# Kernel tuning notes

Measured on AMD Instinct MI355X. Metric: run time of the kernel, lower is better.

The kernel has to match this reference:

```python
import jax, jax.numpy as jnp
import numpy as np

E, K = 8, 2            # num_experts, top_k
H, DFF = 1024, 2048    # embd_dim, d_ff
B, S = 4, 1024


def setup_inputs() -> dict:
    key = jax.random.key(0)
    ks = jax.random.split(key, 5)
    s_in = 1.0 / np.sqrt(H)
    s_ff = 1.0 / np.sqrt(DFF)
    return {
        "x": jax.random.normal(ks[0], (B, S, H), jnp.float32),
        "centroids": jax.random.normal(ks[1], (E, H), jnp.float32),
        # nn.Linear weights are [out, in]
        "gate_w": jax.random.normal(ks[2], (E, DFF, H), jnp.float32) * s_in,
        "up_w": jax.random.normal(ks[3], (E, DFF, H), jnp.float32) * s_in,
        "down_w": jax.random.normal(ks[4], (E, H, DFF), jnp.float32) * s_ff,
        "routing_bias": jnp.zeros((E,), jnp.float32),
    }


def reference(x, centroids, gate_w, up_w, down_w, routing_bias):
    Bb, Ss, Hh = x.shape
    xf = x.reshape(-1, Hh)  # [T, H]
    # sigmoid affinity router + (non-trainable) routing bias
    affinity = jax.nn.sigmoid(xf @ centroids.T)          # [T, E]
    topk_scores, topk_idx = jax.lax.top_k(affinity + routing_bias, K)  # [T, K]
    topk_w = jax.nn.softmax(topk_scores, axis=-1)        # [T, K]

    # Dense per-expert SwiGLU FFN on all tokens (same math as the
    # sort/gather grouped loop; selection happens in the gather below).
    g = jnp.einsum('th,efh->etf', xf, gate_w)            # [E, T, DFF]
    u = jnp.einsum('th,efh->etf', xf, up_w)              # [E, T, DFF]
    y = jnp.einsum('etf,ehf->eth', jax.nn.silu(g) * u, down_w)  # [E, T, H]

    yt = jnp.transpose(y, (1, 0, 2))                     # [T, E, H]
    sel = jnp.take_along_axis(yt, topk_idx[:, :, None], axis=1)  # [T, K, H]
    out_flat = jnp.sum(sel * topk_w[:, :, None], axis=1)  # [T, H]

    counts = jnp.bincount(topk_idx.ravel(), length=E)    # per-expert token counts
    return out_flat.reshape(Bb, Ss, Hh), counts
```

## Files before the change

kernel.cpp:

```cpp
#include <hip/hip_runtime.h>
#include <math.h>

constexpr int E = 8, H = 1024, DFF = 2048, T = 4096;
constexpr int TR = 8192;
constexpr int MAXJ = 72;

typedef __bf16 bf16x8 __attribute__((ext_vector_type(8)));
typedef __bf16 bf16x4 __attribute__((ext_vector_type(4)));
typedef float f32x4 __attribute__((ext_vector_type(4)));

__device__ __forceinline__ void gload16(const void* g, void* l) {
    __builtin_amdgcn_global_load_lds(
        (const __attribute__((address_space(1))) unsigned int*)g,
        (__attribute__((address_space(3))) unsigned int*)l, 16, 0, 0);
}

__global__ __launch_bounds__(256) void k1_affinity(
    const float* __restrict__ x, const float* __restrict__ cent,
    const float* __restrict__ bias,
    int* __restrict__ se, float* __restrict__ sw) {
    __shared__ float cs[E * H];
    int tid = threadIdx.x;
    for (int i = tid; i < E * H / 4; i += 256)
        ((float4*)cs)[i] = ((const float4*)cent)[i];
    __syncthreads();

    int wave = tid >> 6, lane = tid & 63;
    int t = blockIdx.x * 4 + wave;
    const float4* xr = (const float4*)(x + (size_t)t * H);
    float acc[E] = {};
    #pragma unroll
    for (int it = 0; it < 4; it++) {
        float4 xv = xr[lane + it * 64];
        #pragma unroll
        for (int e = 0; e < E; e++) {
            float4 cv = ((const float4*)(cs + e * H))[lane + it * 64];
            acc[e] = fmaf(xv.x, cv.x, acc[e]);
            acc[e] = fmaf(xv.y, cv.y, acc[e]);
            acc[e] = fmaf(xv.z, cv.z, acc[e]);
            acc[e] = fmaf(xv.w, cv.w, acc[e]);
        }
    }
    #pragma unroll
    for (int off = 32; off; off >>= 1)
        #pragma unroll
        for (int e = 0; e < E; e++) acc[e] += __shfl_down(acc[e], off);

    if (lane == 0) {
        float s[E];
        #pragma unroll
        for (int e = 0; e < E; e++)
            s[e] = 1.0f / (1.0f + expf(-acc[e])) + bias[e];
        int i0 = 0;
        for (int e = 1; e < E; e++) if (s[e] > s[i0]) i0 = e;
        int i1 = -1;
        for (int e = 0; e < E; e++) {
            if (e == i0) continue;
            if (i1 < 0 || s[e] > s[i1]) i1 = e;
        }
        float m = fmaxf(s[i0], s[i1]);
        float w0 = expf(s[i0] - m), w1 = expf(s[i1] - m);
        float inv = 1.0f / (w0 + w1);
        se[2 * t] = i0;     sw[2 * t] = w0 * inv;
        se[2 * t + 1] = i1; sw[2 * t + 1] = w1 * inv;
    }
}

__global__ __launch_bounds__(256) void k1b_partition(
    const int* __restrict__ se, int* __restrict__ token_list,
    int* __restrict__ sp, int* __restrict__ cnt) {
    int e = blockIdx.x;
    int tid = threadIdx.x;
    int wave = tid >> 6, lane = tid & 63;
    __shared__ int wsum[4];
    int running = 0;
    for (int c0 = 0; c0 < 2 * T; c0 += 256) {
        int i = c0 + tid;
        bool pred = (se[i] == e);
        unsigned long long mask = __ballot(pred);
        int pos_in_wave = __popcll(mask & ((1ull << lane) - 1ull));
        if (lane == 0) wsum[wave] = __popcll(mask);
        __syncthreads();
        int wbase = 0;
        for (int w2 = 0; w2 < wave; w2++) wbase += wsum[w2];
        int total = wsum[0] + wsum[1] + wsum[2] + wsum[3];
        if (pred) {
            int p = running + wbase + pos_in_wave;
            token_list[e * T + p] = i >> 1;
            sp[i] = p;
        }
        running += total;
        __syncthreads();
    }
    if (tid == 0) cnt[e] = running;
}

__global__ void k15_offsets(const int* __restrict__ cnt, int* __restrict__ off,
                            float* __restrict__ out_counts,
                            int* __restrict__ jobs, int* __restrict__ njobs) {
    if (threadIdx.x == 0) {
        int acc = 0, nj = 0;
        for (int e = 0; e < E; e++) {
            off[e] = acc; acc += cnt[e];
            int mts = (cnt[e] + 127) >> 7;
            for (int mt = 0; mt < mts; mt++) jobs[nj++] = e * 64 + mt;
        }
        njobs[0] = nj;
    }
    if (threadIdx.x < E) out_counts[threadIdx.x] = (float)cnt[threadIdx.x];
}

__global__ __launch_bounds__(256) void k_conv(const float* __restrict__ in,
                                              __bf16* __restrict__ out, int n4) {
    int i = blockIdx.x * 256 + threadIdx.x;
    if (i < n4) {
        float4 v = ((const float4*)in)[i];
        bf16x4 o = {(__bf16)v.x, (__bf16)v.y, (__bf16)v.z, (__bf16)v.w};
        ((bf16x4*)out)[i] = o;
    }
}

__global__ __launch_bounds__(256) void k_conv3(
    const float* __restrict__ gw, __bf16* __restrict__ gwb,
    const float* __restrict__ uw, __bf16* __restrict__ uwb,
    const float* __restrict__ x, __bf16* __restrict__ xb,
    int w4, int x4) {
    int i = blockIdx.x * 256 + threadIdx.x;
    const float* in; __bf16* out; int idx;
    if (i < w4) { in = gw; out = gwb; idx = i; }
    else if (i < 2 * w4) { in = uw; out = uwb; idx = i - w4; }
    else { idx = i - 2 * w4; if (idx >= x4) return; in = x; out = xb; }
    float4 v = ((const float4*)in)[idx];
    bf16x4 o = {(__bf16)v.x, (__bf16)v.y, (__bf16)v.z, (__bf16)v.w};
    ((bf16x4*)out)[idx] = o;
}

__global__ __launch_bounds__(256, 2) void k2_gateup(
    const __bf16* __restrict__ xb, const __bf16* __restrict__ gwb,
    const __bf16* __restrict__ uwb, const int* __restrict__ cnt,
    const int* __restrict__ off, const int* __restrict__ token_list,
    const int* __restrict__ jobs, const int* __restrict__ njobs,
    __bf16* __restrict__ h) {
    int jt = blockIdx.x >> 4, nt = blockIdx.x & 15;
    if (jt >= njobs[0]) return;
    int job = jobs[jt];
    int e = job >> 6, mt = job & 63;
    int Me = cnt[e], offe = off[e];

    __shared__ __bf16 As[128 * 64];
    __shared__ __bf16 Bg[128 * 64];
    __shared__ __bf16 Bu[128 * 64];

    int tid = threadIdx.x;
    int lane = tid & 63, w = tid >> 6;
    int wm = w >> 1, wn = w & 1;

    const __bf16* asrc[4];
    const __bf16 *bsg[4], *bsu[4];
    #pragma unroll
    for (int rr = 0; rr < 4; rr++) {
        int l = rr * 256 + tid;
        int row = l >> 3, sl = l & 7;
        int gr = mt * 128 + row; if (gr >= Me) gr = Me - 1;
        int tok = token_list[e * T + gr];
        asrc[rr] = xb + (size_t)tok * H + ((sl ^ (row & 7)) * 8);
        size_t base = ((size_t)e * DFF + nt * 128 + row) * H + ((sl ^ (row & 7)) * 8);
        bsg[rr] = gwb + base;
        bsu[rr] = uwb + base;
    }

    f32x4 accg[4][4] = {};
    f32x4 accu[4][4] = {};
    int kq = lane >> 4, m15 = lane & 15;

    for (int k0 = 0; k0 < H; k0 += 64) {
        #pragma unroll
        for (int rr = 0; rr < 4; rr++) {
            gload16(asrc[rr] + k0, &As[(rr * 256 + tid) * 8]);
            gload16(bsg[rr] + k0, &Bg[(rr * 256 + tid) * 8]);
            gload16(bsu[rr] + k0, &Bu[(rr * 256 + tid) * 8]);
        }
        __syncthreads();

        #pragma unroll
        for (int kc = 0; kc < 2; kc++) {
            bf16x8 af[4], gf[4], uf[4];
            #pragma unroll
            for (int i = 0; i < 4; i++) {
                int row = wm * 64 + i * 16 + m15;
                int sl = (kc * 4 + kq) ^ (row & 7);
                af[i] = *(const bf16x8*)&As[row * 64 + sl * 8];
            }
            #pragma unroll
            for (int j = 0; j < 4; j++) {
                int row = wn * 64 + j * 16 + m15;
                int sl = (kc * 4 + kq) ^ (row & 7);
                gf[j] = *(const bf16x8*)&Bg[row * 64 + sl * 8];
                uf[j] = *(const bf16x8*)&Bu[row * 64 + sl * 8];
            }
            #pragma unroll
            for (int i = 0; i < 4; i++)
                #pragma unroll
                for (int j = 0; j < 4; j++) {
                    accg[i][j] = __builtin_amdgcn_mfma_f32_16x16x32_bf16(af[i], gf[j], accg[i][j], 0, 0, 0);
                    accu[i][j] = __builtin_amdgcn_mfma_f32_16x16x32_bf16(af[i], uf[j], accu[i][j], 0, 0, 0);
                }
        }
        __syncthreads();
    }

    #pragma unroll
    for (int i = 0; i < 4; i++)
        #pragma unroll
        for (int j = 0; j < 4; j++) {
            int nloc = wn * 64 + j * 16 + m15;
            size_t c = (size_t)nt * 128 + nloc;
            #pragma unroll
            for (int p = 0; p < 4; p++) {
                int mloc = wm * 64 + i * 16 + kq * 4 + p;
                int mrow = mt * 128 + mloc;
                if (mrow < Me) {
                    float g = accg[i][j][p], u = accu[i][j][p];
                    float sig = 1.0f / (1.0f + __expf(-g));
                    h[(size_t)(offe + mrow) * DFF + c] = (__bf16)(g * sig * u);
                }
            }
        }
}

__global__ __launch_bounds__(512, 2) void k3_down(
    const __bf16* __restrict__ h, const __bf16* __restrict__ dwb,
    const int* __restrict__ cnt, const int* __restrict__ off,
    const int* __restrict__ jobs, const int* __restrict__ njobs,
    __bf16* __restrict__ y) {
    int jt = blockIdx.x >> 2, nt = blockIdx.x & 3;
    if (jt >= njobs[0]) return;
    int job = jobs[jt];
    int e = job >> 6, mt = job & 63;
    int Me = cnt[e], offe = off[e];

    __shared__ __bf16 As[128 * 64];
    __shared__ __bf16 Bs[256 * 64];

    int tid = threadIdx.x;
    int lane = tid & 63, w = tid >> 6;
    int wm = w >> 2, wn = w & 3;

    const __bf16* asrc[2];
    #pragma unroll
    for (int rr = 0; rr < 2; rr++) {
        int l = rr * 512 + tid;
        int row = l >> 3, sl = l & 7;
        int koff = (sl ^ (row & 7)) * 8;
        int gr = mt * 128 + row; if (gr >= Me) gr = Me - 1;
        asrc[rr] = h + (size_t)(offe + gr) * DFF + koff;
    }
    const __bf16* bsrc[4];
    #pragma unroll
    for (int rr = 0; rr < 4; rr++) {
        int l = rr * 512 + tid;
        int row = l >> 3, sl = l & 7;
        int koff = (sl ^ (row & 7)) * 8;
        bsrc[rr] = dwb + ((size_t)e * H + nt * 256 + row) * DFF + koff;
    }

    f32x4 acc[4][4] = {};
    int kq = lane >> 4, m15 = lane & 15;

    for (int k0 = 0; k0 < DFF; k0 += 64) {
        #pragma unroll
        for (int rr = 0; rr < 2; rr++)
            gload16(asrc[rr] + k0, &As[(rr * 512 + tid) * 8]);
        #pragma unroll
        for (int rr = 0; rr < 4; rr++)
            gload16(bsrc[rr] + k0, &Bs[(rr * 512 + tid) * 8]);
        __syncthreads();

        #pragma unroll
        for (int kc = 0; kc < 2; kc++) {
            bf16x8 af[4], bf[4];
            #pragma unroll
            for (int i = 0; i < 4; i++) {
                int row = wm * 64 + i * 16 + m15;
                int sl = (kc * 4 + kq) ^ (row & 7);
                af[i] = *(const bf16x8*)&As[row * 64 + sl * 8];
            }
            #pragma unroll
            for (int j = 0; j < 4; j++) {
                int row = wn * 64 + j * 16 + m15;
                int sl = (kc * 4 + kq) ^ (row & 7);
                bf[j] = *(const bf16x8*)&Bs[row * 64 + sl * 8];
            }
            #pragma unroll
            for (int i = 0; i < 4; i++)
                #pragma unroll
                for (int j = 0; j < 4; j++)
                    acc[i][j] = __builtin_amdgcn_mfma_f32_16x16x32_bf16(af[i], bf[j], acc[i][j], 0, 0, 0);
        }
        __syncthreads();
    }

    #pragma unroll
    for (int i = 0; i < 4; i++)
        #pragma unroll
        for (int j = 0; j < 4; j++) {
            int nglob = nt * 256 + wn * 64 + j * 16 + m15;
            #pragma unroll
            for (int p = 0; p < 4; p++) {
                int mloc = wm * 64 + i * 16 + kq * 4 + p;
                int mrow = mt * 128 + mloc;
                if (mrow < Me)
                    y[(size_t)(offe + mrow) * H + nglob] = (__bf16)acc[i][j][p];
            }
        }
}

__global__ __launch_bounds__(256) void k_gather(
    const __bf16* __restrict__ y, const int* __restrict__ se,
    const int* __restrict__ sp, const float* __restrict__ sw,
    const int* __restrict__ off, float* __restrict__ out) {
    int t = blockIdx.x;
    int r0 = off[se[2 * t]] + sp[2 * t];
    int r1 = off[se[2 * t + 1]] + sp[2 * t + 1];
    float w0 = sw[2 * t], w1 = sw[2 * t + 1];
    const bf16x4* y0 = (const bf16x4*)(y + (size_t)r0 * H);
    const bf16x4* y1 = (const bf16x4*)(y + (size_t)r1 * H);
    float4* o = (float4*)(out + (size_t)t * H);
    int c = threadIdx.x;
    bf16x4 a = y0[c], b = y1[c];
    float4 v;
    v.x = w0 * (float)a[0] + w1 * (float)b[0];
    v.y = w0 * (float)a[1] + w1 * (float)b[1];
    v.z = w0 * (float)a[2] + w1 * (float)b[2];
    v.w = w0 * (float)a[3] + w1 * (float)b[3];
    o[c] = v;
}

extern "C" void kernel_launch(void* const* d_in, const int* in_sizes, int n_in,
                              void* d_out, int out_size, void* d_ws, size_t ws_size,
                              hipStream_t stream) {
    const float* x    = (const float*)d_in[0];
    const float* cent = (const float*)d_in[1];
    const float* gw   = (const float*)d_in[2];
    const float* uw   = (const float*)d_in[3];
    const float* dw   = (const float*)d_in[4];
    const float* bias = (const float*)d_in[5];
    float* out = (float*)d_out;

    char* ws = (char*)d_ws;
    int*   cnt        = (int*)(ws + 0);
    int*   off        = (int*)(ws + 64);
    int*   se         = (int*)(ws + 128);
    int*   sp         = (int*)(ws + 128 + 32768);
    float* sw         = (float*)(ws + 128 + 65536);
    int*   token_list = (int*)(ws + 128 + 98304);
    int*   jobs       = (int*)(ws + 229504);
    int*   njobs      = (int*)(ws + 229824);
    const size_t MB = 1u << 20;
    __bf16* gwb = (__bf16*)(ws + 1 * MB);
    __bf16* uwb = (__bf16*)(ws + 1 * MB + 33554432);
    __bf16* dwb = gwb;
    __bf16* y   = uwb;
    __bf16* xb  = (__bf16*)(ws + 1 * MB + 67108864);
    __bf16* h   = (__bf16*)(ws + 1 * MB + 75497472);

    const int W4 = E * DFF * H / 4;
    const int X4 = T * H / 4;
    const int C3 = 2 * W4 + X4;

    k_conv3<<<(C3 + 255) / 256, 256, 0, stream>>>(gw, gwb, uw, uwb, x, xb, W4, X4);
    k1_affinity<<<T / 4, 256, 0, stream>>>(x, cent, bias, se, sw);
    k1b_partition<<<E, 256, 0, stream>>>(se, token_list, sp, cnt);
    k15_offsets<<<1, 64, 0, stream>>>(cnt, off, out + (size_t)T * H, jobs, njobs);
    k2_gateup<<<MAXJ * 16, 256, 0, stream>>>(xb, gwb, uwb, cnt, off, token_list, jobs, njobs, h);
    k_conv<<<(W4 + 255) / 256, 256, 0, stream>>>(dw, dwb, W4);
    k3_down<<<MAXJ * 4, 512, 0, stream>>>(h, dwb, cnt, off, jobs, njobs, y);
    k_gather<<<T, 256, 0, stream>>>(y, se, sp, sw, off, out);
}
```

Before: 389.8 us.

## Double-buffer LDS in both expert GEMMs and retile gate/up and down

Both grouped GEMM kernels now double-buffer their shared-memory tiles, so the global-to-LDS loads for the next K step are issued before computing on the current one. This aims to hide load latency behind MFMA work. The gate/up kernel moves to 256-row token tiles with 512 threads, using a separate job list built at 256-row granularity. The down kernel moves to 128x128 tiles with 256 threads and more N tiles per job. The larger LDS footprint (about 128KB per block in gate/up) limits occupancy to about one block per CU, and the larger M tiles add padding waste on experts with partial tiles.

```diff
diff --git a/kernel.cpp b/kernel.cpp
--- a/kernel.cpp
+++ b/kernel.cpp
@@ -3,7 +3,8 @@
 
 constexpr int E = 8, H = 1024, DFF = 2048, T = 4096;
 constexpr int TR = 8192;
-constexpr int MAXJ = 72;
+constexpr int MAXJ2 = TR / 256 + E;
+constexpr int MAXJ3 = TR / 128 + E;
 
 typedef __bf16 bf16x8 __attribute__((ext_vector_type(8)));
 typedef __bf16 bf16x4 __attribute__((ext_vector_type(4)));
@@ -97,15 +98,19 @@
 
 __global__ void k15_offsets(const int* __restrict__ cnt, int* __restrict__ off,
                             float* __restrict__ out_counts,
-                            int* __restrict__ jobs, int* __restrict__ njobs) {
+                            int* __restrict__ jobs2, int* __restrict__ jobs3,
+                            int* __restrict__ njobs) {
     if (threadIdx.x == 0) {
-        int acc = 0, nj = 0;
+        int acc = 0, nj2 = 0, nj3 = 0;
         for (int e = 0; e < E; e++) {
             off[e] = acc; acc += cnt[e];
-            int mts = (cnt[e] + 127) >> 7;
-            for (int mt = 0; mt < mts; mt++) jobs[nj++] = e * 64 + mt;
-        }
-        njobs[0] = nj;
+            int m2 = (cnt[e] + 255) >> 8;
+            for (int mt = 0; mt < m2; mt++) jobs2[nj2++] = e * 64 + mt;
+            int m3 = (cnt[e] + 127) >> 7;
+            for (int mt = 0; mt < m3; mt++) jobs3[nj3++] = e * 64 + mt;
+        }
+        njobs[0] = nj2;
+        njobs[1] = nj3;
     }
     if (threadIdx.x < E) out_counts[threadIdx.x] = (float)cnt[threadIdx.x];
 }
@@ -135,7 +140,7 @@
     ((bf16x4*)out)[idx] = o;
 }
 
-__global__ __launch_bounds__(256, 2) void k2_gateup(
+__global__ __launch_bounds__(512, 2) void k2_gateup(
     const __bf16* __restrict__ xb, const __bf16* __restrict__ gwb,
     const __bf16* __restrict__ uwb, const int* __restrict__ cnt,
     const int* __restrict__ off, const int* __restrict__ token_list,
@@ -147,23 +152,28 @@
     int e = job >> 6, mt = job & 63;
     int Me = cnt[e], offe = off[e];
 
-    __shared__ __bf16 As[128 * 64];
-    __shared__ __bf16 Bg[128 * 64];
-    __shared__ __bf16 Bu[128 * 64];
+    __shared__ __bf16 As[2][256 * 64];
+    __shared__ __bf16 Bg[2][128 * 64];
+    __shared__ __bf16 Bu[2][128 * 64];
 
     int tid = threadIdx.x;
     int lane = tid & 63, w = tid >> 6;
     int wm = w >> 1, wn = w & 1;
 
     const __bf16* asrc[4];
-    const __bf16 *bsg[4], *bsu[4];
+    const __bf16 *bsg[2], *bsu[2];
     #pragma unroll
     for (int rr = 0; rr < 4; rr++) {
-        int l = rr * 256 + tid;
+        int l = rr * 512 + tid;
         int row = l >> 3, sl = l & 7;
-        int gr = mt * 128 + row; if (gr >= Me) gr = Me - 1;
+        int gr = mt * 256 + row; if (gr >= Me) gr = Me - 1;
         int tok = token_list[e * T + gr];
         asrc[rr] = xb + (size_t)tok * H + ((sl ^ (row & 7)) * 8);
+    }
+    #pragma unroll
+    for (int rr = 0; rr < 2; rr++) {
+        int l = rr * 512 + tid;
+        int row = l >> 3, sl = l & 7;
         size_t base = ((size_t)e * DFF + nt * 128 + row) * H + ((sl ^ (row & 7)) * 8);
         bsg[rr] = gwb + base;
         bsu[rr] = uwb + base;
@@ -173,14 +183,25 @@
     f32x4 accu[4][4] = {};
     int kq = lane >> 4, m15 = lane & 15;
 
+    #pragma unroll
+    for (int rr = 0; rr < 4; rr++) gload16(asrc[rr], &As[0][(rr * 512 + tid) * 8]);
+    #pragma unroll
+    for (int rr = 0; rr < 2; rr++) gload16(bsg[rr], &Bg[0][(rr * 512 + tid) * 8]);
+    #pragma unroll
+    for (int rr = 0; rr < 2; rr++) gload16(bsu[rr], &Bu[0][(rr * 512 + tid) * 8]);
+    __syncthreads();
+
+    int cur = 0;
     for (int k0 = 0; k0 < H; k0 += 64) {
-        #pragma unroll
-        for (int rr = 0; rr < 4; rr++) {
-            gload16(asrc[rr] + k0, &As[(rr * 256 + tid) * 8]);
-            gload16(bsg[rr] + k0, &Bg[(rr * 256 + tid) * 8]);
-            gload16(bsu[rr] + k0, &Bu[(rr * 256 + tid) * 8]);
-        }
-        __syncthreads();
+        if (k0 + 64 < H) {
+            int nb = cur ^ 1, kn = k0 + 64;
+            #pragma unroll
+            for (int rr = 0; rr < 4; rr++) gload16(asrc[rr] + kn, &As[nb][(rr * 512 + tid) * 8]);
+            #pragma unroll
+            for (int rr = 0; rr < 2; rr++) gload16(bsg[rr] + kn, &Bg[nb][(rr * 512 + tid) * 8]);
+            #pragma unroll
+            for (int rr = 0; rr < 2; rr++) gload16(bsu[rr] + kn, &Bu[nb][(rr * 512 + tid) * 8]);
+        }
 
         #pragma unroll
         for (int kc = 0; kc < 2; kc++) {
@@ -189,14 +210,14 @@
             for (int i = 0; i < 4; i++) {
                 int row = wm * 64 + i * 16 + m15;
                 int sl = (kc * 4 + kq) ^ (row & 7);
-                af[i] = *(const bf16x8*)&As[row * 64 + sl * 8];
+                af[i] = *(const bf16x8*)&As[cur][row * 64 + sl * 8];
             }
             #pragma unroll
             for (int j = 0; j < 4; j++) {
                 int row = wn * 64 + j * 16 + m15;
                 int sl = (kc * 4 + kq) ^ (row & 7);
-                gf[j] = *(const bf16x8*)&Bg[row * 64 + sl * 8];
-                uf[j] = *(const bf16x8*)&Bu[row * 64 + sl * 8];
+                gf[j] = *(const bf16x8*)&Bg[cur][row * 64 + sl * 8];
+                uf[j] = *(const bf16x8*)&Bu[cur][row * 64 + sl * 8];
             }
             #pragma unroll
             for (int i = 0; i < 4; i++)
@@ -207,6 +228,7 @@
                 }
         }
         __syncthreads();
+        cur ^= 1;
     }
 
     #pragma unroll
@@ -218,7 +240,7 @@
             #pragma unroll
             for (int p = 0; p < 4; p++) {
                 int mloc = wm * 64 + i * 16 + kq * 4 + p;
-                int mrow = mt * 128 + mloc;
+                int mrow = mt * 256 + mloc;
                 if (mrow < Me) {
                     float g = accg[i][j][p], u = accu[i][j][p];
                     float sig = 1.0f / (1.0f + __expf(-g));
@@ -228,53 +250,54 @@
         }
 }
 
-__global__ __launch_bounds__(512, 2) void k3_down(
+__global__ __launch_bounds__(256, 2) void k3_down(
     const __bf16* __restrict__ h, const __bf16* __restrict__ dwb,
     const int* __restrict__ cnt, const int* __restrict__ off,
     const int* __restrict__ jobs, const int* __restrict__ njobs,
     __bf16* __restrict__ y) {
-    int jt = blockIdx.x >> 2, nt = blockIdx.x & 3;
-    if (jt >= njobs[0]) return;
+    int jt = blockIdx.x >> 3, nt = blockIdx.x & 7;
+    if (jt >= njobs[1]) return;
     int job = jobs[jt];
     int e = job >> 6, mt = job & 63;
     int Me = cnt[e], offe = off[e];
 
-    __shared__ __bf16 As[128 * 64];
-    __shared__ __bf16 Bs[256 * 64];
+    __shared__ __bf16 As[2][128 * 64];
+    __shared__ __bf16 Bs[2][128 * 64];
 
     int tid = threadIdx.x;
     int lane = tid & 63, w = tid >> 6;
-    int wm = w >> 2, wn = w & 3;
-
-    const __bf16* asrc[2];
-    #pragma unroll
-    for (int rr = 0; rr < 2; rr++) {
-        int l = rr * 512 + tid;
+    int wm = w >> 1, wn = w & 1;
+
+    const __bf16* asrc[4];
+    const __bf16* bsrc[4];
+    #pragma unroll
+    for (int rr = 0; rr < 4; rr++) {
+        int l = rr * 256 + tid;
         int row = l >> 3, sl = l & 7;
         int koff = (sl ^ (row & 7)) * 8;
         int gr = mt * 128 + row; if (gr >= Me) gr = Me - 1;
         asrc[rr] = h + (size_t)(offe + gr) * DFF + koff;
-    }
-    const __bf16* bsrc[4];
-    #pragma unroll
-    for (int rr = 0; rr < 4; rr++) {
-        int l = rr * 512 + tid;
-        int row = l >> 3, sl = l & 7;
-        int koff = (sl ^ (row & 7)) * 8;
-        bsrc[rr] = dwb + ((size_t)e * H + nt * 256 + row) * DFF + koff;
+        bsrc[rr] = dwb + ((size_t)e * H + nt * 128 + row) * DFF + koff;
     }
 
     f32x4 acc[4][4] = {};
     int kq = lane >> 4, m15 = lane & 15;
 
+    #pragma unroll
+    for (int rr = 0; rr < 4; rr++) gload16(asrc[rr], &As[0][(rr * 256 + tid) * 8]);
+    #pragma unroll
+    for (int rr = 0; rr < 4; rr++) gload16(bsrc[rr], &Bs[0][(rr * 256 + tid) * 8]);
+    __syncthreads();
+
+    int cur = 0;
     for (int k0 = 0; k0 < DFF; k0 += 64) {
-        #pragma unroll
-        for (int rr = 0; rr < 2; rr++)
-            gload16(asrc[rr] + k0, &As[(rr * 512 + tid) * 8]);
-        #pragma unroll
-        for (int rr = 0; rr < 4; rr++)
-            gload16(bsrc[rr] + k0, &Bs[(rr * 512 + tid) * 8]);
-        __syncthreads();
+        if (k0 + 64 < DFF) {
+            int nb = cur ^ 1, kn = k0 + 64;
+            #pragma unroll
+            for (int rr = 0; rr < 4; rr++) gload16(asrc[rr] + kn, &As[nb][(rr * 256 + tid) * 8]);
+            #pragma unroll
+            for (int rr = 0; rr < 4; rr++) gload16(bsrc[rr] + kn, &Bs[nb][(rr * 256 + tid) * 8]);
+        }
 
         #pragma unroll
         for (int kc = 0; kc < 2; kc++) {
@@ -283,13 +306,13 @@
             for (int i = 0; i < 4; i++) {
                 int row = wm * 64 + i * 16 + m15;
                 int sl = (kc * 4 + kq) ^ (row & 7);
-                af[i] = *(const bf16x8*)&As[row * 64 + sl * 8];
+                af[i] = *(const bf16x8*)&As[cur][row * 64 + sl * 8];
             }
             #pragma unroll
             for (int j = 0; j < 4; j++) {
                 int row = wn * 64 + j * 16 + m15;
                 int sl = (kc * 4 + kq) ^ (row & 7);
-                bf[j] = *(const bf16x8*)&Bs[row * 64 + sl * 8];
+                bf[j] = *(const bf16x8*)&Bs[cur][row * 64 + sl * 8];
             }
             #pragma unroll
             for (int i = 0; i < 4; i++)
@@ -298,13 +321,14 @@
                     acc[i][j] = __builtin_amdgcn_mfma_f32_16x16x32_bf16(af[i], bf[j], acc[i][j], 0, 0, 0);
         }
         __syncthreads();
+        cur ^= 1;
     }
 
     #pragma unroll
     for (int i = 0; i < 4; i++)
         #pragma unroll
         for (int j = 0; j < 4; j++) {
-            int nglob = nt * 256 + wn * 64 + j * 16 + m15;
+            int nglob = nt * 128 + wn * 64 + j * 16 + m15;
             #pragma unroll
             for (int p = 0; p < 4; p++) {
                 int mloc = wm * 64 + i * 16 + kq * 4 + p;
@@ -354,8 +378,9 @@
     int*   sp         = (int*)(ws + 128 + 32768);
     float* sw         = (float*)(ws + 128 + 65536);
     int*   token_list = (int*)(ws + 128 + 98304);
-    int*   jobs       = (int*)(ws + 229504);
-    int*   njobs      = (int*)(ws + 229824);
+    int*   jobs2      = (int*)(ws + 229504);
+    int*   jobs3      = (int*)(ws + 229760);
+    int*   njobs      = (int*)(ws + 230400);
     const size_t MB = 1u << 20;
     __bf16* gwb = (__bf16*)(ws + 1 * MB);
     __bf16* uwb = (__bf16*)(ws + 1 * MB + 33554432);
@@ -371,9 +396,9 @@
     k_conv3<<<(C3 + 255) / 256, 256, 0, stream>>>(gw, gwb, uw, uwb, x, xb, W4, X4);
     k1_affinity<<<T / 4, 256, 0, stream>>>(x, cent, bias, se, sw);
     k1b_partition<<<E, 256, 0, stream>>>(se, token_list, sp, cnt);
-    k15_offsets<<<1, 64, 0, stream>>>(cnt, off, out + (size_t)T * H, jobs, njobs);
-    k2_gateup<<<MAXJ * 16, 256, 0, stream>>>(xb, gwb, uwb, cnt, off, token_list, jobs, njobs, h);
+    k15_offsets<<<1, 64, 0, stream>>>(cnt, off, out + (size_t)T * H, jobs2, jobs3, njobs);
+    k2_gateup<<<MAXJ2 * 16, 512, 0, stream>>>(xb, gwb, uwb, cnt, off, token_list, jobs2, njobs, h);
     k_conv<<<(W4 + 255) / 256, 256, 0, stream>>>(dw, dwb, W4);
-    k3_down<<<MAXJ * 4, 512, 0, stream>>>(h, dwb, cnt, off, jobs, njobs, y);
+    k3_down<<<MAXJ3 * 8, 256, 0, stream>>>(h, dwb, cnt, off, jobs3, njobs, y);
     k_gather<<<T, 256, 0, stream>>>(y, se, sp, sw, off, out);
 }
```

New measurement: 425.6 us. +9.2%, slower.
